# Kernel tuning notes

Measured on AMD Instinct MI355X. Metric: run time of the kernel, lower is better.

Reference implementation:

```python
import jax, jax.numpy as jnp
import numpy as np

TAU = 1.0  # gumbel_temp
EPS = 1e-10


def setup_inputs() -> dict:
    key = jax.random.key(0)
    k1, k2, k3 = jax.random.split(key, 3)
    B, T, D, K = 8, 1024, 256, 4096
    z = jax.random.normal(k1, (B, T, D), dtype=jnp.float32)
    u = jax.random.uniform(k2, (B, T, K), dtype=jnp.float32)
    codebook = jax.random.normal(k3, (K, D), dtype=jnp.float32)
    codebook_usage = jnp.zeros((K,), dtype=jnp.float32)
    return {"z": z, "u": u, "codebook": codebook, "codebook_usage": codebook_usage}


def reference(z, u, codebook, codebook_usage):
    B, T, D = z.shape
    K = codebook.shape[0]

    # squared-distance matrix: ||z||^2 + ||e||^2 - 2 z.e  -> [B,T,K]
    z_sq = jnp.sum(z * z, axis=-1, keepdims=True)           # [B,T,1]
    e_sq = jnp.sum(codebook * codebook, axis=-1)            # [K]
    dot = jnp.einsum('btd,kd->btk', z, codebook)            # [B,T,K]
    distances = z_sq + e_sq - 2.0 * dot

    # gumbel-softmax straight-through (training path)
    logits = -distances
    gumbel = -jnp.log(-jnp.log(u + EPS) + EPS)
    soft = jax.nn.softmax((logits + gumbel) / TAU, axis=-1)
    indices = jnp.argmax(soft, axis=-1)                     # [B,T]
    hard = jax.nn.one_hot(indices, K, dtype=soft.dtype)
    codes = hard - jax.lax.stop_gradient(soft) + soft

    quantized = jnp.einsum('btk,kd->btd', codes, codebook)
    embedding = codebook[indices]                           # [B,T,D]

    # straight-through quantized output + commitment loss
    z_q = z + jax.lax.stop_gradient(quantized - z)
    commitment = jnp.mean(jnp.square(jax.lax.stop_gradient(z_q) - z))

    # usage update (EMA buffer math that feeds entropy/perplexity outputs)
    n_i = jnp.zeros((K,), z.dtype).at[indices.reshape(-1)].add(1.0)
    usage = codebook_usage * 0.99 + n_i
    usage_sum = jnp.sum(usage)
    usage_prob = jnp.where(usage_sum > 0, usage / (usage_sum + EPS), jnp.full_like(usage, 1.0 / K))
    entropy = -jnp.sum(usage_prob * jnp.log(usage_prob + EPS))
    perplexity = jnp.exp(entropy)

    return (z_q, embedding, indices, commitment, perplexity, entropy)
```

## Files before the change

### kernel.cpp

```cpp
#include <hip/hip_runtime.h>
#include <math.h>

#define NTOK 8192
#define DDIM 256
#define KCB  4096
#define GEPS 1e-10f

typedef __attribute__((ext_vector_type(8))) short short8;
typedef __attribute__((ext_vector_type(8))) unsigned short ushort8;
typedef __attribute__((ext_vector_type(4))) float f32x4;

#define WS_ESQ  0
#define WS_ZSQ  (WS_ESQ + KCB)
#define WS_KEY  (WS_ZSQ + NTOK)
#define WS_HIST (WS_KEY + 2 * NTOK)
#define WS_COMM (WS_HIST + KCB)
#define WS_ZH   32776
#define WS_END  (WS_ZH + (3 * NTOK * DDIM + 3 * KCB * DDIM) / 2)

#define PO_Z  (NTOK * DDIM)
#define PO_C  (KCB * DDIM)
#define PO_CB (3 * NTOK * DDIM)

#define OUT_ZQ   0
#define OUT_EMB  (NTOK * DDIM)
#define OUT_IDX  (2 * NTOK * DDIM)
#define OUT_SCAL (2 * NTOK * DDIM + NTOK)

__device__ __forceinline__ unsigned short f2bf(float x) {
  unsigned int u = __float_as_uint(x);
  u += 0x7FFFu + ((u >> 16) & 1u);
  return (unsigned short)(u >> 16);
}
__device__ __forceinline__ float bf2f(unsigned short h) {
  return __uint_as_float(((unsigned int)h) << 16);
}

__device__ __forceinline__ void gload16(const void* g, void* l) {
  __builtin_amdgcn_global_load_lds(
      (const __attribute__((address_space(1))) unsigned int*)g,
      (__attribute__((address_space(3))) unsigned int*)l, 16, 0, 0);
}

__global__ __launch_bounds__(256) void k_prep(const float* __restrict__ cb,
                                              const float* __restrict__ z,
                                              float* __restrict__ esq,
                                              float* __restrict__ zsq,
                                              float* __restrict__ keyf,
                                              float* __restrict__ hist,
                                              float* __restrict__ comm,
                                              unsigned short* __restrict__ zh) {
  const int l   = threadIdx.x & 63;
  const int wid = threadIdx.x >> 6;
  const int r0  = blockIdx.x * 64 + wid * 16;
  const int rl  = r0 + (l >> 2);
  const bool isc = rl < KCB;
  const int r_in  = isc ? rl : rl - KCB;
  const int r0_in = isc ? r0 : r0 - KCB;
  const float* src = isc ? (cb + (size_t)rl * DDIM) : (z + (size_t)r_in * DDIM);
  const int ss = l & 3;
  const int dh = ss ^ ((r_in >> 2) & 3);
  const unsigned NR      = isc ? (unsigned)KCB : (unsigned)NTOK;
  const unsigned pbase   = isc ? (unsigned)PO_CB : 0u;
  const unsigned pstride = isc ? (unsigned)PO_C : (unsigned)PO_Z;

  float ssum = 0.0f;
  #pragma unroll
  for (int kk = 0; kk < 8; ++kk) {
    const float4 va = *(const float4*)(src + kk * 32 + dh * 8);
    const float4 vb = *(const float4*)(src + kk * 32 + dh * 8 + 4);
    ssum += va.x * va.x + va.y * va.y + va.z * va.z + va.w * va.w
          + vb.x * vb.x + vb.y * vb.y + vb.z * vb.z + vb.w * vb.w;
    if (zh) {
      const float vv[8] = {va.x, va.y, va.z, va.w, vb.x, vb.y, vb.z, vb.w};
      ushort8 h8, m8, l8;
      #pragma unroll
      for (int e = 0; e < 8; ++e) {
        const float x  = vv[e];
        const unsigned short h = f2bf(x);
        const float r1 = x - bf2f(h);
        const unsigned short m = f2bf(r1);
        const float r2 = r1 - bf2f(m);
        h8[e] = h; m8[e] = m; l8[e] = f2bf(r2);
      }
      const unsigned off = pbase + (unsigned)kk * NR * 32 + (unsigned)r0_in * 32
                         + (unsigned)l * 8;
      *(ushort8*)(zh + off)                = h8;
      *(ushort8*)(zh + off + pstride)      = m8;
      *(ushort8*)(zh + off + 2 * pstride)  = l8;
    }
  }
  ssum += __shfl_xor(ssum, 1);
  ssum += __shfl_xor(ssum, 2);
  if ((l & 3) == 0) {
    if (isc) esq[rl] = ssum;
    else     zsq[r_in] = ssum;
  }

  const int gid = blockIdx.x * 256 + threadIdx.x;
  if (gid < 2 * NTOK) keyf[gid] = 0.0f;
  else if (gid < 2 * NTOK + KCB) hist[gid - 2 * NTOK] = 0.0f;
  else if (gid == 2 * NTOK + KCB) comm[0] = 0.0f;
}

__global__ __launch_bounds__(256, 2) void k_mfma(const unsigned short* __restrict__ zh,
                                                 const float* __restrict__ u,
                                                 const float* __restrict__ esq,
                                                 const float* __restrict__ zsq,
                                                 unsigned long long* __restrict__ key) {
  __shared__ __align__(1024) unsigned char lbuf[49152];

  const int tid = threadIdx.x;
  const int l   = tid & 63;
  const int wid = tid >> 6;

  const int bid = blockIdx.x;
  const int s   = (bid & 7) * 256 + (bid >> 3);
  const int cx  = ((s >> 8) << 2) + (s & 3);
  const int cy  = (s & 255) >> 2;
  const int tok0 = cy * 128;
  const int c0   = cx * 128;

  const int lrow = l & 15;
  const int lkg  = l >> 4;
  const int tw = (wid >> 1) * 64;
  const int cw = (wid & 1) * 64;

  unsigned int srcoff[12], lbase[12];
  #pragma unroll
  for (int j = 0; j < 12; ++j) {
    const int c = wid + 4 * j;
    unsigned int off, lb;
    if (j < 6) {
      const int p = c >> 3, sub = c & 7;
      off = (unsigned)p * PO_Z + (unsigned)tok0 * 32 + (unsigned)sub * 512;
      lb  = (unsigned)(p * 8192 + sub * 1024);
    } else {
      const int q = c - 24;
      const int p = q >> 3, sub = q & 7;
      off = (unsigned)PO_CB + (unsigned)p * PO_C + (unsigned)c0 * 32
          + (unsigned)sub * 512;
      lb  = (unsigned)(24576 + p * 8192 + sub * 1024);
    }
    srcoff[j] = off + (unsigned)l * 8;
    lbase[j]  = lb;
  }

  f32x4 acc[4][4] = {};
  const unsigned int sw = ((unsigned int)(lkg ^ ((lrow >> 2) & 3))) << 4;
  const int rb = lkg * 4;

  #pragma unroll
  for (int j = 0; j < 6; ++j)  gload16(zh + srcoff[j], lbuf + lbase[j]);
  #pragma unroll
  for (int j = 6; j < 12; ++j) gload16(zh + srcoff[j], lbuf + lbase[j]);

  #pragma unroll
  for (int kk = 0; kk < 8; ++kk) {
    asm volatile("s_waitcnt vmcnt(0)" ::: "memory");
    __builtin_amdgcn_sched_barrier(0);
    __builtin_amdgcn_s_barrier();
    __builtin_amdgcn_sched_barrier(0);

    short8 ah[4], am[4], al[4], bh[4], bm[4], bl[4];
    #pragma unroll
    for (int ni = 0; ni < 4; ++ni) {
      const unsigned int boff = (unsigned int)(cw + ni * 16 + lrow) * 64 + sw;
      bh[ni] = *(const short8*)(lbuf + 24576 + boff);
      bm[ni] = *(const short8*)(lbuf + 32768 + boff);
      bl[ni] = *(const short8*)(lbuf + 40960 + boff);
    }
    #pragma unroll
    for (int mi = 0; mi < 4; ++mi) {
      const unsigned int aoff = (unsigned int)(tw + mi * 16 + lrow) * 64 + sw;
      ah[mi] = *(const short8*)(lbuf + 0     + aoff);
      am[mi] = *(const short8*)(lbuf + 8192  + aoff);
      al[mi] = *(const short8*)(lbuf + 16384 + aoff);
    }

    asm volatile("s_waitcnt lgkmcnt(0)" ::: "memory");
    __builtin_amdgcn_sched_barrier(0);
    __builtin_amdgcn_s_barrier();
    __builtin_amdgcn_sched_barrier(0);

    if (kk < 7) {
      const unsigned int ka = (unsigned)(kk + 1) * (NTOK * 32);
      const unsigned int kb = (unsigned)(kk + 1) * (KCB * 32);
      #pragma unroll
      for (int j = 0; j < 6; ++j)  gload16(zh + srcoff[j] + ka, lbuf + lbase[j]);
      #pragma unroll
      for (int j = 6; j < 12; ++j) gload16(zh + srcoff[j] + kb, lbuf + lbase[j]);
    }
    __builtin_amdgcn_sched_barrier(0);

    __builtin_amdgcn_s_setprio(1);
    #pragma unroll
    for (int mi = 0; mi < 4; ++mi) {
      #pragma unroll
      for (int ni = 0; ni < 4; ++ni) {
        f32x4 a = acc[mi][ni];
        a = __builtin_amdgcn_mfma_f32_16x16x32_bf16(am[mi], bm[ni], a, 0, 0, 0);
        a = __builtin_amdgcn_mfma_f32_16x16x32_bf16(ah[mi], bl[ni], a, 0, 0, 0);
        a = __builtin_amdgcn_mfma_f32_16x16x32_bf16(al[mi], bh[ni], a, 0, 0, 0);
        a = __builtin_amdgcn_mfma_f32_16x16x32_bf16(ah[mi], bm[ni], a, 0, 0, 0);
        a = __builtin_amdgcn_mfma_f32_16x16x32_bf16(am[mi], bh[ni], a, 0, 0, 0);
        a = __builtin_amdgcn_mfma_f32_16x16x32_bf16(ah[mi], bh[ni], a, 0, 0, 0);
        acc[mi][ni] = a;
      }
    }
    __builtin_amdgcn_s_setprio(0);
    __builtin_amdgcn_sched_barrier(0);
  }

  float esv[4];
  #pragma unroll
  for (int ni = 0; ni < 4; ++ni) esv[ni] = esq[c0 + cw + ni * 16 + lrow];

  #pragma unroll
  for (int mi = 0; mi < 4; ++mi) {
    #pragma unroll
    for (int r = 0; r < 4; ++r) {
      const int t  = tok0 + tw + mi * 16 + rb + r;
      const float zq = zsq[t];
      float bv = -3.402823e38f;
      int   bc = c0 + cw + lrow;
      #pragma unroll
      for (int ni = 0; ni < 4; ++ni) {
        const int c = c0 + cw + ni * 16 + lrow;
        const float uu = u[(size_t)t * KCB + c];
        const float g  = -logf(-logf(uu + GEPS) + GEPS);
        const float sc = -((zq + esv[ni]) - 2.0f * acc[mi][ni][r]) + g;
        if (sc > bv) { bv = sc; bc = c; }
      }
      #pragma unroll
      for (int m = 1; m < 16; m <<= 1) {
        const float ov = __shfl_xor(bv, m);
        const int   oc = __shfl_xor(bc, m);
        if (ov > bv || (ov == bv && oc < bc)) { bv = ov; bc = oc; }
      }
      if (lrow == 0) {
        unsigned int b = __float_as_uint(bv);
        b = (b & 0x80000000u) ? ~b : (b | 0x80000000u);
        const unsigned long long kk2 =
            ((unsigned long long)b << 32) | (unsigned int)(KCB - 1 - bc);
        atomicMax(&key[t], kk2);
      }
    }
  }
}

#define BT 128
#define BK 128
#define DC 32
#define PS 132
__global__ __launch_bounds__(256) void k_score(const float* __restrict__ z,
                                               const float* __restrict__ u,
                                               const float* __restrict__ cb,
                                               const float* __restrict__ esq,
                                               const float* __restrict__ zsq,
                                               unsigned long long* __restrict__ key) {
  __shared__ float zsm[DC][PS];
  __shared__ float csm[DC][PS];
  const int tid  = threadIdx.x;
  const int tok0 = blockIdx.x * BT;
  const int kb   = blockIdx.y * BK;
  const int tx = tid & 15;
  const int ty = tid >> 4;
  const int srow = tid >> 3;
  const int sc4  = (tid & 7) * 4;
  float acc[8][8] = {};
  float4 zr[4], cr[4];
  #pragma unroll
  for (int j = 0; j < 4; ++j) {
    const int r = srow + 32 * j;
    zr[j] = *(const float4*)(z  + (size_t)(tok0 + r) * DDIM + sc4);
    cr[j] = *(const float4*)(cb + (size_t)(kb  + r) * DDIM + sc4);
  }
  for (int dc = 0; dc < DDIM / DC; ++dc) {
    __syncthreads();
    #pragma unroll
    for (int j = 0; j < 4; ++j) {
      const int r = srow + 32 * j;
      zsm[sc4 + 0][r] = zr[j].x; zsm[sc4 + 1][r] = zr[j].y;
      zsm[sc4 + 2][r] = zr[j].z; zsm[sc4 + 3][r] = zr[j].w;
      csm[sc4 + 0][r] = cr[j].x; csm[sc4 + 1][r] = cr[j].y;
      csm[sc4 + 2][r] = cr[j].z; csm[sc4 + 3][r] = cr[j].w;
    }
    __syncthreads();
    if (dc + 1 < DDIM / DC) {
      const int d0 = (dc + 1) * DC;
      #pragma unroll
      for (int j = 0; j < 4; ++j) {
        const int r = srow + 32 * j;
        zr[j] = *(const float4*)(z  + (size_t)(tok0 + r) * DDIM + d0 + sc4);
        cr[j] = *(const float4*)(cb + (size_t)(kb  + r) * DDIM + d0 + sc4);
      }
    }
    #pragma unroll 4
    for (int d = 0; d < DC; ++d) {
      const float4 za = *(const float4*)&zsm[d][8 * ty];
      const float4 zb = *(const float4*)&zsm[d][8 * ty + 4];
      const float4 ca = *(const float4*)&csm[d][8 * tx];
      const float4 cc = *(const float4*)&csm[d][8 * tx + 4];
      const float zf[8] = {za.x, za.y, za.z, za.w, zb.x, zb.y, zb.z, zb.w};
      const float cf[8] = {ca.x, ca.y, ca.z, ca.w, cc.x, cc.y, cc.z, cc.w};
      #pragma unroll
      for (int i = 0; i < 8; ++i)
        #pragma unroll
        for (int j = 0; j < 8; ++j) acc[i][j] += zf[i] * cf[j];
    }
  }
  const float4 ea = *(const float4*)(esq + kb + 8 * tx);
  const float4 eb = *(const float4*)(esq + kb + 8 * tx + 4);
  const float esa[8] = {ea.x, ea.y, ea.z, ea.w, eb.x, eb.y, eb.z, eb.w};
  float bv[8]; int bj[8];
  #pragma unroll
  for (int i = 0; i < 8; ++i) {
    const int tok = tok0 + 8 * ty + i;
    const float zq = zsq[tok];
    const float4 ua = *(const float4*)(u + (size_t)tok * KCB + kb + 8 * tx);
    const float4 ub = *(const float4*)(u + (size_t)tok * KCB + kb + 8 * tx + 4);
    const float uu[8] = {ua.x, ua.y, ua.z, ua.w, ub.x, ub.y, ub.z, ub.w};
    bv[i] = -3.402823e38f; bj[i] = kb + 8 * tx;
    #pragma unroll
    for (int j = 0; j < 8; ++j) {
      const float g = -logf(-logf(uu[j] + GEPS) + GEPS);
      const float s = -((zq + esa[j]) - 2.0f * acc[i][j]) + g;
      if (s > bv[i]) { bv[i] = s; bj[i] = kb + 8 * tx + j; }
    }
  }
  __syncthreads();
  float* pv = &zsm[0][0];
  int*   pi = (int*)&csm[0][0];
  #pragma unroll
  for (int i = 0; i < 8; ++i) {
    pv[(8 * ty + i) * 16 + tx] = bv[i];
    pi[(8 * ty + i) * 16 + tx] = bj[i];
  }
  __syncthreads();
  if (tid < BT) {
    float best  = pv[tid * 16];
    int   besti = pi[tid * 16];
    for (int x = 1; x < 16; ++x) {
      const float v = pv[tid * 16 + x];
      if (v > best) { best = v; besti = pi[tid * 16 + x]; }
    }
    unsigned int b = __float_as_uint(best);
    b = (b & 0x80000000u) ? ~b : (b | 0x80000000u);
    const unsigned long long kk =
        ((unsigned long long)b << 32) | (unsigned int)(KCB - 1 - besti);
    atomicMax(&key[tok0 + tid], kk);
  }
}

__global__ __launch_bounds__(256) void k_final(const float* __restrict__ z,
                                               const float* __restrict__ cb,
                                               const unsigned long long* __restrict__ key,
                                               float* __restrict__ out,
                                               float* __restrict__ hist,
                                               float* __restrict__ comm) {
  __shared__ float cred[4];
  const int lane = threadIdx.x & 63;
  const int wv   = threadIdx.x >> 6;
  const int tok  = blockIdx.x * 4 + wv;
  const unsigned long long kk = key[tok];
  int bi = KCB - 1 - (int)(kk & 0xFFFFFFFFu);
  bi = min(max(bi, 0), KCB - 1);
  const float4 c  = *(const float4*)(cb + (size_t)bi * DDIM + 4 * lane);
  const float4 zv = *(const float4*)(z + (size_t)tok * DDIM + 4 * lane);
  float4 q;
  q.x = zv.x + (c.x - zv.x);
  q.y = zv.y + (c.y - zv.y);
  q.z = zv.z + (c.z - zv.z);
  q.w = zv.w + (c.w - zv.w);
  const size_t o = (size_t)tok * DDIM + 4 * lane;
  *(float4*)(out + OUT_ZQ  + o) = q;
  *(float4*)(out + OUT_EMB + o) = c;
  const float dx = q.x - zv.x, dy = q.y - zv.y, dz = q.z - zv.z, dw = q.w - zv.w;
  float s = dx * dx + dy * dy + dz * dz + dw * dw;
  #pragma unroll
  for (int o2 = 32; o2 > 0; o2 >>= 1) s += __shfl_down(s, o2);
  if (lane == 0) {
    cred[wv] = s;
    atomicAdd(&hist[bi], 1.0f);
    out[OUT_IDX + tok] = (float)bi;
  }
  __syncthreads();
  if (threadIdx.x == 0)
    atomicAdd(comm, (cred[0] + cred[1]) + (cred[2] + cred[3]));
}

__global__ __launch_bounds__(1024) void k_scal(const float* __restrict__ cu,
                                               const float* __restrict__ hist,
                                               const float* __restrict__ comm,
                                               float* __restrict__ out) {
  __shared__ float red[1024];
  const int tid = threadIdx.x;
  float us[4];
  float s = 0.0f;
  #pragma unroll
  for (int j = 0; j < 4; ++j) {
    const int k = tid * 4 + j;
    us[j] = cu[k] * 0.99f + hist[k];
    s += us[j];
  }
  red[tid] = s; __syncthreads();
  for (int o = 512; o > 0; o >>= 1) {
    if (tid < o) red[tid] += red[tid + o];
    __syncthreads();
  }
  const float usum = red[0];
  __syncthreads();
  float e = 0.0f;
  #pragma unroll
  for (int j = 0; j < 4; ++j) {
    const float p = (usum > 0.0f) ? (us[j] / (usum + GEPS)) : (1.0f / (float)KCB);
    e -= p * logf(p + GEPS);
  }
  red[tid] = e; __syncthreads();
  for (int o = 512; o > 0; o >>= 1) {
    if (tid < o) red[tid] += red[tid + o];
    __syncthreads();
  }
  if (tid == 0) {
    const float entropy = red[0];
    out[OUT_SCAL + 0] = comm[0] / (float)((size_t)NTOK * DDIM);
    out[OUT_SCAL + 1] = expf(entropy);
    out[OUT_SCAL + 2] = entropy;
  }
}

extern "C" void kernel_launch(void* const* d_in, const int* in_sizes, int n_in,
                              void* d_out, int out_size, void* d_ws, size_t ws_size,
                              hipStream_t stream) {
  const float* z  = (const float*)d_in[0];
  const float* u  = (const float*)d_in[1];
  const float* cb = (const float*)d_in[2];
  const float* cu = (const float*)d_in[3];

  float* ws   = (float*)d_ws;
  float* esq  = ws + WS_ESQ;
  float* zsq  = ws + WS_ZSQ;
  float* keyf = ws + WS_KEY;
  unsigned long long* key = (unsigned long long*)keyf;
  float* hist = ws + WS_HIST;
  float* comm = ws + WS_COMM;
  float* out  = (float*)d_out;

  if (ws_size >= (size_t)WS_END * 4) {
    unsigned short* zh = (unsigned short*)(ws + WS_ZH);
    k_prep<<<dim3((KCB + NTOK) / 64), dim3(256), 0, stream>>>(
        cb, z, esq, zsq, keyf, hist, comm, zh);
    k_mfma<<<dim3(2048), dim3(256), 0, stream>>>(zh, u, esq, zsq, key);
  } else {
    k_prep<<<dim3((KCB + NTOK) / 64), dim3(256), 0, stream>>>(
        cb, z, esq, zsq, keyf, hist, comm, (unsigned short*)nullptr);
    k_score<<<dim3(NTOK / BT, KCB / BK), dim3(256), 0, stream>>>(z, u, cb, esq, zsq, key);
  }

  k_final<<<dim3(NTOK / 4), dim3(256), 0, stream>>>(z, cb, key, out, hist, comm);
  k_scal <<<dim3(1), dim3(1024), 0, stream>>>(cu, hist, comm, out);
}
```

Measured before the change: 176.8 us.

## Drop software prefetch pipeline and raise occupancy to three blocks per CU

The GEMM main loop no longer overlaps the next k-slice global-to-LDS copy with the current MFMA work. Each iteration now loads, synchronizes, then computes, and A fragments are read per row tile to cut register pressure. Launch bounds go from 2 to 3 blocks per CU, so latency hiding relies on more resident blocks rather than intra-block pipelining. The 48KB of LDS per block may still limit how many blocks fit, and removing the prefetch and setprio exposes memory latency inside each block.

```diff
diff --git a/kernel.cpp b/kernel.cpp
--- a/kernel.cpp
+++ b/kernel.cpp
@@ -103,7 +103,7 @@
   else if (gid == 2 * NTOK + KCB) comm[0] = 0.0f;
 }
 
-__global__ __launch_bounds__(256, 2) void k_mfma(const unsigned short* __restrict__ zh,
+__global__ __launch_bounds__(256, 3) void k_mfma(const unsigned short* __restrict__ zh,
                                                  const float* __restrict__ u,
                                                  const float* __restrict__ esq,
                                                  const float* __restrict__ zsq,
@@ -150,66 +150,42 @@
   const unsigned int sw = ((unsigned int)(lkg ^ ((lrow >> 2) & 3))) << 4;
   const int rb = lkg * 4;
 
-  #pragma unroll
-  for (int j = 0; j < 6; ++j)  gload16(zh + srcoff[j], lbuf + lbase[j]);
-  #pragma unroll
-  for (int j = 6; j < 12; ++j) gload16(zh + srcoff[j], lbuf + lbase[j]);
-
-  #pragma unroll
   for (int kk = 0; kk < 8; ++kk) {
-    asm volatile("s_waitcnt vmcnt(0)" ::: "memory");
-    __builtin_amdgcn_sched_barrier(0);
-    __builtin_amdgcn_s_barrier();
-    __builtin_amdgcn_sched_barrier(0);
-
-    short8 ah[4], am[4], al[4], bh[4], bm[4], bl[4];
+    const unsigned int ka = (unsigned)kk * (NTOK * 32);
+    const unsigned int kb = (unsigned)kk * (KCB * 32);
+    __syncthreads();
+    #pragma unroll
+    for (int j = 0; j < 6; ++j)  gload16(zh + srcoff[j] + ka, lbuf + lbase[j]);
+    #pragma unroll
+    for (int j = 6; j < 12; ++j) gload16(zh + srcoff[j] + kb, lbuf + lbase[j]);
+    __syncthreads();
+
+    short8 bfr[3][4];
     #pragma unroll
     for (int ni = 0; ni < 4; ++ni) {
       const unsigned int boff = (unsigned int)(cw + ni * 16 + lrow) * 64 + sw;
-      bh[ni] = *(const short8*)(lbuf + 24576 + boff);
-      bm[ni] = *(const short8*)(lbuf + 32768 + boff);
-      bl[ni] = *(const short8*)(lbuf + 40960 + boff);
+      bfr[0][ni] = *(const short8*)(lbuf + 24576 + boff);
+      bfr[1][ni] = *(const short8*)(lbuf + 32768 + boff);
+      bfr[2][ni] = *(const short8*)(lbuf + 40960 + boff);
     }
     #pragma unroll
     for (int mi = 0; mi < 4; ++mi) {
       const unsigned int aoff = (unsigned int)(tw + mi * 16 + lrow) * 64 + sw;
-      ah[mi] = *(const short8*)(lbuf + 0     + aoff);
-      am[mi] = *(const short8*)(lbuf + 8192  + aoff);
-      al[mi] = *(const short8*)(lbuf + 16384 + aoff);
-    }
-
-    asm volatile("s_waitcnt lgkmcnt(0)" ::: "memory");
-    __builtin_amdgcn_sched_barrier(0);
-    __builtin_amdgcn_s_barrier();
-    __builtin_amdgcn_sched_barrier(0);
-
-    if (kk < 7) {
-      const unsigned int ka = (unsigned)(kk + 1) * (NTOK * 32);
-      const unsigned int kb = (unsigned)(kk + 1) * (KCB * 32);
-      #pragma unroll
-      for (int j = 0; j < 6; ++j)  gload16(zh + srcoff[j] + ka, lbuf + lbase[j]);
-      #pragma unroll
-      for (int j = 6; j < 12; ++j) gload16(zh + srcoff[j] + kb, lbuf + lbase[j]);
-    }
-    __builtin_amdgcn_sched_barrier(0);
-
-    __builtin_amdgcn_s_setprio(1);
-    #pragma unroll
-    for (int mi = 0; mi < 4; ++mi) {
+      const short8 ah = *(const short8*)(lbuf + 0     + aoff);
+      const short8 am = *(const short8*)(lbuf + 8192  + aoff);
+      const short8 al = *(const short8*)(lbuf + 16384 + aoff);
       #pragma unroll
       for (int ni = 0; ni < 4; ++ni) {
         f32x4 a = acc[mi][ni];
-        a = __builtin_amdgcn_mfma_f32_16x16x32_bf16(am[mi], bm[ni], a, 0, 0, 0);
-        a = __builtin_amdgcn_mfma_f32_16x16x32_bf16(ah[mi], bl[ni], a, 0, 0, 0);
-        a = __builtin_amdgcn_mfma_f32_16x16x32_bf16(al[mi], bh[ni], a, 0, 0, 0);
-        a = __builtin_amdgcn_mfma_f32_16x16x32_bf16(ah[mi], bm[ni], a, 0, 0, 0);
-        a = __builtin_amdgcn_mfma_f32_16x16x32_bf16(am[mi], bh[ni], a, 0, 0, 0);
-        a = __builtin_amdgcn_mfma_f32_16x16x32_bf16(ah[mi], bh[ni], a, 0, 0, 0);
+        a = __builtin_amdgcn_mfma_f32_16x16x32_bf16(am, bfr[1][ni], a, 0, 0, 0);
+        a = __builtin_amdgcn_mfma_f32_16x16x32_bf16(ah, bfr[2][ni], a, 0, 0, 0);
+        a = __builtin_amdgcn_mfma_f32_16x16x32_bf16(al, bfr[0][ni], a, 0, 0, 0);
+        a = __builtin_amdgcn_mfma_f32_16x16x32_bf16(ah, bfr[1][ni], a, 0, 0, 0);
+        a = __builtin_amdgcn_mfma_f32_16x16x32_bf16(am, bfr[0][ni], a, 0, 0, 0);
+        a = __builtin_amdgcn_mfma_f32_16x16x32_bf16(ah, bfr[0][ni], a, 0, 0, 0);
         acc[mi][ni] = a;
       }
     }
-    __builtin_amdgcn_s_setprio(0);
-    __builtin_amdgcn_sched_barrier(0);
   }
 
   float esv[4];
```

New measurement: 163.4 us, median of 2. -7.6%, faster.
